# Optimization experiments

Hardware: AMD Instinct MI355X
Metric: run time of the kernel (lower is better)

The kernel has to match this reference:

```python
import jax, jax.numpy as jnp
import numpy as np

N, C, NUM_IDS = 4096, 2048, 256


def setup_inputs() -> dict:
    key = jax.random.key(0)
    k1, k2 = jax.random.split(key)
    x = jax.random.normal(k1, (N, C), dtype=jnp.float32)
    target = jax.random.randint(k2, (N,), 0, NUM_IDS, dtype=jnp.int64)
    return {
        "input": x,
        "target": target,
        "hyper_paramter": 1,
        "usemean": 1,
        "use_exp": 0,
    }


def _pair_stats(x, W):
    """Vectorized sum over lower-tri pairs (i>j) weighted by W (lower-triangular 0/1).

    cov = sum_{i>j} W_ij (x_i - x_j)(x_i - x_j)^T = X^T (diag(S 1) - S) X, S = W + W^T
    vec = sum_{i>j} W_ij (x_i - x_j)       = X^T (rowsum(W) - colsum(W))
    """
    S = W + W.T                       # [N, N] symmetric pair mask
    d = S.sum(axis=1)                 # degree
    Lx = d[:, None] * x - S @ x       # (diag(d) - S) @ X, [N, C]
    cov = x.T @ Lx                    # [C, C]
    vec = x.T @ (W.sum(axis=1) - W.sum(axis=0))  # [C]
    return cov, vec, W.sum()


def reference(input, target, hyper_paramter, usemean, use_exp):
    x = input
    same_id = (target[:, None] == target[None, :])
    pos_l = jnp.tril(same_id.astype(x.dtype), -1)          # positive pairs, i>j
    neg_l = jnp.tril((~same_id).astype(x.dtype), -1)       # negative pairs, i>j

    cov_i, sum_i, npos = _pair_stats(x, pos_l)
    cov_j, sum_j, nneg = _pair_stats(x, neg_l)

    norm_i = jnp.linalg.norm(cov_i)
    norm_j = jnp.linalg.norm(cov_j)

    if use_exp:
        dist = jnp.exp(-jnp.linalg.norm(cov_i - cov_j))
        loss = dist
    else:
        # original broadcasts zeros(C) + diff(C,1) -> (C,C) matrix of identical
        # columns; its Frobenius norm = sqrt(C) * norm(column vector)
        mean_norm = jnp.sqrt(jnp.asarray(x.shape[1], x.dtype)) * jnp.linalg.norm(
            sum_i / npos - sum_j / nneg
        )
        dist = norm_i - hyper_paramter * norm_j - usemean * mean_norm
        loss = jnp.maximum(dist, 0.0)
    return (loss, dist, norm_i, norm_j)
```

## Files before the change

### kernel.cpp

```cpp
#include <hip/hip_runtime.h>
#include <math.h>


#define N_ROWS 4096
#define C_DIM  2048
#define NCLS   256
#define RLCAP  96
#define NRB    17
#define NKS    32
#define TSB    16384
#define SLOT_B 32768

typedef __attribute__((ext_vector_type(4))) float f32x4;
typedef __attribute__((ext_vector_type(2))) long v2i64;

__device__ __forceinline__ void gload16(const void* g, void* l) {
    __builtin_amdgcn_global_load_lds(
        (const __attribute__((address_space(1))) unsigned int*)g,
        (__attribute__((address_space(3))) unsigned int*)l, 16, 0, 0);
}

__device__ __forceinline__ int pk4_fp8(float a, float b, float c, float d) {
    int r = __builtin_amdgcn_cvt_pk_fp8_f32(a, b, 0, false);
    r = __builtin_amdgcn_cvt_pk_fp8_f32(c, d, r, true);
    return r;
}

__global__ __launch_bounds__(256) void k_scan_conv(
    const int* __restrict__ t, const float* __restrict__ x,
    float* __restrict__ ca, float* __restrict__ cb,
    float* __restrict__ dr, float* __restrict__ nposf,
    unsigned char* __restrict__ xbf) {
    __shared__ int ts[N_ROWS];
    __shared__ int rl[RLCAP];
    __shared__ int cnt_s;
    int a = blockIdx.x, tid = threadIdx.x;
    for (int i = tid; i < N_ROWS; i += 256) ts[i] = t[i];
    __syncthreads();
    if (tid < 64) {
        int lane = tid;
        unsigned long long ltmask = (1ULL << lane) - 1ULL;
        int base = 0;
        for (int i0 = 0; i0 < N_ROWS; i0 += 64) {
            int i = i0 + lane;
            bool m = (ts[i] == a);
            unsigned long long mask = __ballot(m);
            if (m) {
                int r = base + (int)__popcll(mask & ltmask);
                if (r < RLCAP) rl[r] = i;
            }
            base += (int)__popcll(mask);
        }
        if (lane == 0) {
            cnt_s = base;
            float cf = (float)base;
            atomicAdd(nposf, 0.5f * cf * (cf - 1.f));
        }
        int cc = base < RLCAP ? base : RLCAP;
        for (int r = lane; r < cc; r += 64) {
            int i = rl[r];
            ca[i] = (float)(2 * r - base + 1);
            cb[i] = (float)(2 * i - 2 * r + base - N_ROWS);
            dr[i] = (float)base;
        }
    }
    __syncthreads();
    int cnt = cnt_s < RLCAP ? cnt_s : RLCAP;
    int c0 = tid * 4, c1 = 1024 + tid * 4;
    float s0=0,s1=0,s2=0,s3=0,s4=0,s5=0,s6=0,s7=0;
    int ks0 = c0 >> 6, cc0 = c0 & 63;
    int ks1 = c1 >> 6, cc1 = c1 & 63;
    int sl0 = (cc0 & 31) >> 3, ch0 = cc0 >> 5, b0 = cc0 & 7;
    int sl1 = (cc1 & 31) >> 3, ch1 = cc1 >> 5, b1 = cc1 & 7;
    for (int r = 0; r < cnt; ++r) {
        int i = rl[r];
        const float* row = x + (size_t)i * C_DIM;
        float4 v0 = *(const float4*)(row + c0);
        float4 v1 = *(const float4*)(row + c1);
        s0+=v0.x; s1+=v0.y; s2+=v0.z; s3+=v0.w;
        s4+=v1.x; s5+=v1.y; s6+=v1.z; s7+=v1.w;
        int rb2 = i >> 8, rr = i & 255;
        unsigned char* tb = xbf + (size_t)rb2 * NKS * TSB;
        int w0 = pk4_fp8(v0.x, v0.y, v0.z, v0.w);
        int w1 = pk4_fp8(v1.x, v1.y, v1.z, v1.w);
        int sz = (rr >> 1) & 3;
        *(int*)(tb + (size_t)ks0 * TSB + rr * 64 + (((sl0 ^ sz) << 4) + (ch0 << 3) + b0)) = w0;
        *(int*)(tb + (size_t)ks1 * TSB + rr * 64 + (((sl1 ^ sz) << 4) + (ch1 << 3) + b1)) = w1;
    }
    unsigned char* tbg = xbf + (size_t)16 * NKS * TSB;
    int g0 = pk4_fp8(s0, s1, s2, s3);
    int g1 = pk4_fp8(s4, s5, s6, s7);
    int sza = (a >> 1) & 3;
    *(int*)(tbg + (size_t)ks0 * TSB + a * 64 + (((sl0 ^ sza) << 4) + (ch0 << 3) + b0)) = g0;
    *(int*)(tbg + (size_t)ks1 * TSB + a * 64 + (((sl1 ^ sza) << 4) + (ch1 << 3) + b1)) = g1;
}

__device__ __forceinline__ v2i64 frag16(const unsigned char* buf, int row0,
                                        int lane) {
    int r = row0 + (lane & 15);
    int s = lane >> 4;
    return *(const v2i64*)(buf + r * 64 + ((s ^ ((r >> 1) & 3)) << 4));
}

__global__ __launch_bounds__(1024, 4) void k_gram(
    const unsigned char* __restrict__ xbf, const float* __restrict__ dr,
    const float* __restrict__ ca, const float* __restrict__ cb,
    const float* __restrict__ nposf, float* __restrict__ ssq) {
    const int nwg = NRB * (NRB + 1) / 2;
    int orig = blockIdx.x;
    int q8 = nwg >> 3, r8 = nwg & 7;
    int xcd = orig & 7, loc = orig >> 3;
    int b = (xcd < r8 ? xcd * (q8 + 1) : r8 * (q8 + 1) + (xcd - r8) * q8) + loc;
    int bi = 0;
    while (b >= NRB - bi) { b -= NRB - bi; ++bi; }
    int bj = bi + b;
    bool diag = (bi == bj);
    bool needRS = (bj == NRB - 1);

    __shared__ __align__(16) unsigned char Sl[4][SLOT_B];
    __shared__ float drow[256], dcol[256], urow[256], ucol[256];
    __shared__ float rsum[256];
    __shared__ float wred[16 * 16];

    int tid = threadIdx.x;
    int lane = tid & 63;
    int w = tid >> 6;
    int wr4 = w >> 2;
    int wc4 = w & 3;

    const unsigned char* abase = xbf + (size_t)bi * NKS * TSB;
    const unsigned char* bbase = xbf + (size_t)bj * NKS * TSB;
    int off0 = w * 1024 + lane * 16;

#pragma unroll
    for (int p = 0; p < 2; ++p) {
        gload16(abase + (size_t)p * TSB + off0, Sl[p] + off0);
        gload16(bbase + (size_t)p * TSB + off0, Sl[p] + 16384 + off0);
    }
    if (tid < 256) {
        float np = nposf[0];
        float inp = 1.f / np;
        float inn = 1.f / (0.5f * (float)N_ROWS * ((float)N_ROWS - 1.f) - np);
        int gi = bi * 256 + tid;
        bool vi = gi < N_ROWS;
        drow[tid] = vi ? dr[gi] : 0.f;
        urow[tid] = vi ? (ca[gi] * inp - cb[gi] * inn) : 0.f;
        int gj = bj * 256 + tid;
        bool vj = gj < N_ROWS;
        dcol[tid] = vj ? dr[gj] : 0.f;
        ucol[tid] = vj ? (ca[gj] * inp - cb[gj] * inn) : 0.f;
        rsum[tid] = 0.f;
    }

    f32x4 acc[4][4] = {};
    __syncthreads();

#define STAGE_STEP(ks)                                                         \
    {                                                                          \
        unsigned char* sl = Sl[(ks) & 3];                                      \
        gload16(abase + (size_t)(ks) * TSB + off0, sl + off0);                 \
        gload16(bbase + (size_t)(ks) * TSB + off0, sl + 16384 + off0);         \
    }

#define COMPUTE_STEP(t)                                                        \
    {                                                                          \
        const unsigned char* sb = Sl[(t) & 3];                                 \
        v2i64 A[4], B[4];                                                      \
        _Pragma("unroll")                                                      \
        for (int m = 0; m < 4; ++m) A[m] = frag16(sb, wr4 * 64 + m * 16, lane);\
        _Pragma("unroll")                                                      \
        for (int n = 0; n < 4; ++n) B[n] = frag16(sb + 16384, wc4 * 64 + n * 16, lane);\
        __builtin_amdgcn_s_setprio(1);                                         \
        _Pragma("unroll")                                                      \
        for (int m = 0; m < 4; ++m)                                            \
            _Pragma("unroll")                                                  \
            for (int n = 0; n < 4; ++n) {                                      \
                acc[m][n] = __builtin_amdgcn_mfma_f32_16x16x32_fp8_fp8(        \
                    A[m][0], B[n][0], acc[m][n], 0, 0, 0);                     \
                acc[m][n] = __builtin_amdgcn_mfma_f32_16x16x32_fp8_fp8(        \
                    A[m][1], B[n][1], acc[m][n], 0, 0, 0);                     \
            }                                                                  \
        __builtin_amdgcn_s_setprio(0);                                         \
    }

    for (int t = 0; t < NKS - 2; ++t) {
        STAGE_STEP(t + 2);
        asm volatile("s_waitcnt vmcnt(4)" ::: "memory");
        asm volatile("s_barrier" ::: "memory");
        COMPUTE_STEP(t);
    }
    asm volatile("s_waitcnt vmcnt(2)" ::: "memory");
    asm volatile("s_barrier" ::: "memory");
    COMPUTE_STEP(NKS - 2);
    asm volatile("s_waitcnt vmcnt(0)" ::: "memory");
    asm volatile("s_barrier" ::: "memory");
    COMPUTE_STEP(NKS - 1);

    float fK = diag ? 1.f : 2.f;
    float vs[7] = {0,0,0,0,0,0,0};
#pragma unroll
    for (int m = 0; m < 4; ++m) {
#pragma unroll
        for (int qq = 0; qq < 4; ++qq) {
            int iw = wr4 * 64 + m * 16 + (lane >> 4) * 4 + qq;
            int gi = bi * 256 + iw;
            float di = drow[iw];
            float ui = urow[iw];
            bool iX = gi < N_ROWS;
            float rs = 0.f;
#pragma unroll
            for (int n = 0; n < 4; ++n) {
                int jw = wc4 * 64 + n * 16 + (lane & 15);
                int gj = bj * 256 + jw;
                float dj = dcol[jw];
                float k = acc[m][n][qq];
                float k2 = k * k;
                bool jX = gj < N_ROWS;
                if (iX && jX) {
                    vs[0] += fK * k2;
                    vs[1] += 0.5f * fK * (di + dj) * k2;
                    vs[2] += fK * di * dj * k2;
                    vs[6] += fK * ui * ucol[jw] * k;
                } else if (iX) {
                    vs[3] += k2;
                    vs[4] += di * k2;
                } else if (!jX) {
                    vs[5] += fK * k2;
                }
                if (needRS) rs += k;
            }
            if (needRS) {
                rs += __shfl_xor(rs, 1);
                rs += __shfl_xor(rs, 2);
                rs += __shfl_xor(rs, 4);
                rs += __shfl_xor(rs, 8);
                if ((lane & 15) == 0) atomicAdd(&rsum[iw], rs);
            }
        }
    }
#pragma unroll
    for (int v = 0; v < 7; ++v) {
        float xv = vs[v];
        for (int off = 32; off; off >>= 1) xv += __shfl_down(xv, off);
        if (lane == 0) wred[w * 16 + v] = xv;
    }
    __syncthreads();
    if (tid < 7) {
        float sum = 0.f;
#pragma unroll
        for (int ww = 0; ww < 16; ++ww) sum += wred[ww * 16 + tid];
        atomicAdd(ssq + (tid == 6 ? 10 : tid), sum);
    }
    if (needRS && tid < 256) {
        float r = rsum[tid];
        float a6 = diag ? 0.f : r * r;
        float a7 = diag ? 0.f : drow[tid] * r * r;
        float a8 = diag ? r * r : 0.f;
        float a9 = diag ? r : 0.f;
        for (int off = 32; off; off >>= 1) {
            a6 += __shfl_down(a6, off);
            a7 += __shfl_down(a7, off);
            a8 += __shfl_down(a8, off);
            a9 += __shfl_down(a9, off);
        }
        if (lane == 0) {
            atomicAdd(ssq + 6, a6);
            atomicAdd(ssq + 7, a7);
            atomicAdd(ssq + 8, a8);
            atomicAdd(ssq + 9, a9);
        }
    }
#undef STAGE_STEP
#undef COMPUTE_STEP
}

__global__ void k_final(const float* __restrict__ ssq, const float* __restrict__ nposf,
                        const int* __restrict__ hyper, const int* __restrict__ usemean,
                        const int* __restrict__ use_exp, float* __restrict__ out) {
    if (threadIdx.x != 0) return;
    double S0 = ssq[0], S1 = ssq[1], S2 = ssq[2], R2 = ssq[3], PG = ssq[4];
    double Q2 = ssq[5], TS = ssq[6], PS = ssq[7], GS = ssq[8], SS = ssq[9];
    double U2 = ssq[10];
    double Nf = (double)N_ROWS;
    double ni2 = S2 - 2.0 * PG + Q2;
    double nj2 = Nf * Nf * S0 + S2 + SS * SS + Q2 - 2.0 * Nf * S1
               - 2.0 * Nf * TS + 2.0 * Nf * R2 + 2.0 * PS - 2.0 * PG - 2.0 * GS;
    double trAB = Nf * S1 - S2 - PS + 2.0 * PG - Nf * R2 + GS - Q2;
    double d2 = ni2 - 2.0 * trAB + nj2;
    float norm_i = (float)sqrt(fmax(ni2, 0.0));
    float norm_j = (float)sqrt(fmax(nj2, 0.0));
    float h = (float)hyper[0], um = (float)usemean[0];
    float loss, dist;
    if (use_exp[0]) {
        dist = (float)exp(-sqrt(fmax(d2, 0.0)));
        loss = dist;
    } else {
        float mean_norm = sqrtf((float)C_DIM) * sqrtf(fmaxf((float)U2, 0.f));
        dist = norm_i - h * norm_j - um * mean_norm;
        loss = fmaxf(dist, 0.f);
    }
    out[0] = loss; out[1] = dist; out[2] = norm_i; out[3] = norm_j;
}

extern "C" void kernel_launch(void* const* d_in, const int* in_sizes, int n_in,
                              void* d_out, int out_size, void* d_ws, size_t ws_size,
                              hipStream_t stream) {
    const float* x = (const float*)d_in[0];
    const int* t = (const int*)d_in[1];
    const int* hyper = (const int*)d_in[2];
    const int* usemean = (const int*)d_in[3];
    const int* use_exp = (const int*)d_in[4];
    float* out = (float*)d_out;

    unsigned char* xbf = (unsigned char*)d_ws;
    size_t xbf_bytes = (size_t)NRB * NKS * TSB;
    float* ca    = (float*)(xbf + xbf_bytes);
    float* cb    = ca + N_ROWS;
    float* dr    = cb + N_ROWS;
    float* ssq   = dr + N_ROWS;
    float* nposf = ssq + 16;

    hipMemsetAsync(ssq, 0, 32 * sizeof(float), stream);

    k_scan_conv<<<NCLS, 256, 0, stream>>>(t, x, ca, cb, dr, nposf, xbf);
    k_gram<<<NRB * (NRB + 1) / 2, 1024, 0, stream>>>(xbf, dr, ca, cb, nposf, ssq);
    k_final<<<1, 64, 0, stream>>>(ssq, nposf, hyper, usemean, use_exp, out);
}
```

Baseline: 79.97 us.

## Split class scan and fp8 conversion into separate kernels with doubled row parallelism

The fused scan+convert kernel is split into a single-wave scan kernel that writes per-class row lists to global memory, a conversion kernel that uses two blocks per class and processes alternating rows, and a small kernel that sums the two partial class sums and packs them to fp8. This doubles the block count for the memory-bound fp32-to-fp8 conversion and drops the 256-thread staging of all targets into shared memory. The cost is two extra kernel launches and a global round trip for the row lists and partial sums.

Result: slower. 96.69 us (+20.9%).

```diff
diff --git a/kernel.cpp b/kernel.cpp
--- a/kernel.cpp
+++ b/kernel.cpp
@@ -26,54 +26,54 @@
     return r;
 }
 
-__global__ __launch_bounds__(256) void k_scan_conv(
-    const int* __restrict__ t, const float* __restrict__ x,
-    float* __restrict__ ca, float* __restrict__ cb,
-    float* __restrict__ dr, float* __restrict__ nposf,
+__global__ __launch_bounds__(64) void k_scan(
+    const int* __restrict__ t, int* __restrict__ counts,
+    int* __restrict__ rowlist, float* __restrict__ ca, float* __restrict__ cb,
+    float* __restrict__ dr, float* __restrict__ nposf) {
+    __shared__ int rl[RLCAP];
+    int a = blockIdx.x;
+    int lane = threadIdx.x;
+    unsigned long long ltmask = (1ULL << lane) - 1ULL;
+    int base = 0;
+    for (int i0 = 0; i0 < N_ROWS; i0 += 64) {
+        int i = i0 + lane;
+        bool m = (t[i] == a);
+        unsigned long long mask = __ballot(m);
+        if (m) {
+            int r = base + (int)__popcll(mask & ltmask);
+            if (r < RLCAP) { rl[r] = i; rowlist[a * RLCAP + r] = i; }
+        }
+        base += (int)__popcll(mask);
+    }
+    if (lane == 0) {
+        counts[a] = base;
+        float cf = (float)base;
+        atomicAdd(nposf, 0.5f * cf * (cf - 1.f));
+    }
+    __syncthreads();
+    int cc = base < RLCAP ? base : RLCAP;
+    for (int r = lane; r < cc; r += 64) {
+        int i = rl[r];
+        ca[i] = (float)(2 * r - base + 1);
+        cb[i] = (float)(2 * i - 2 * r + base - N_ROWS);
+        dr[i] = (float)base;
+    }
+}
+
+__global__ __launch_bounds__(256) void k_conv2(
+    const float* __restrict__ x, const int* __restrict__ counts,
+    const int* __restrict__ rowlist, float* __restrict__ gpart,
     unsigned char* __restrict__ xbf) {
-    __shared__ int ts[N_ROWS];
-    __shared__ int rl[RLCAP];
-    __shared__ int cnt_s;
-    int a = blockIdx.x, tid = threadIdx.x;
-    for (int i = tid; i < N_ROWS; i += 256) ts[i] = t[i];
-    __syncthreads();
-    if (tid < 64) {
-        int lane = tid;
-        unsigned long long ltmask = (1ULL << lane) - 1ULL;
-        int base = 0;
-        for (int i0 = 0; i0 < N_ROWS; i0 += 64) {
-            int i = i0 + lane;
-            bool m = (ts[i] == a);
-            unsigned long long mask = __ballot(m);
-            if (m) {
-                int r = base + (int)__popcll(mask & ltmask);
-                if (r < RLCAP) rl[r] = i;
-            }
-            base += (int)__popcll(mask);
-        }
-        if (lane == 0) {
-            cnt_s = base;
-            float cf = (float)base;
-            atomicAdd(nposf, 0.5f * cf * (cf - 1.f));
-        }
-        int cc = base < RLCAP ? base : RLCAP;
-        for (int r = lane; r < cc; r += 64) {
-            int i = rl[r];
-            ca[i] = (float)(2 * r - base + 1);
-            cb[i] = (float)(2 * i - 2 * r + base - N_ROWS);
-            dr[i] = (float)base;
-        }
-    }
-    __syncthreads();
-    int cnt = cnt_s < RLCAP ? cnt_s : RLCAP;
+    int a = blockIdx.x >> 1, h = blockIdx.x & 1, tid = threadIdx.x;
+    int cnt = counts[a]; if (cnt > RLCAP) cnt = RLCAP;
     int c0 = tid * 4, c1 = 1024 + tid * 4;
     float s0=0,s1=0,s2=0,s3=0,s4=0,s5=0,s6=0,s7=0;
     int ks0 = c0 >> 6, cc0 = c0 & 63;
     int ks1 = c1 >> 6, cc1 = c1 & 63;
     int sl0 = (cc0 & 31) >> 3, ch0 = cc0 >> 5, b0 = cc0 & 7;
     int sl1 = (cc1 & 31) >> 3, ch1 = cc1 >> 5, b1 = cc1 & 7;
-    for (int r = 0; r < cnt; ++r) {
-        int i = rl[r];
+    for (int r = h; r < cnt; r += 2) {
+        int i = rowlist[a * RLCAP + r];
         const float* row = x + (size_t)i * C_DIM;
         float4 v0 = *(const float4*)(row + c0);
         float4 v1 = *(const float4*)(row + c1);
@@ -87,10 +87,29 @@
         *(int*)(tb + (size_t)ks0 * TSB + rr * 64 + (((sl0 ^ sz) << 4) + (ch0 << 3) + b0)) = w0;
         *(int*)(tb + (size_t)ks1 * TSB + rr * 64 + (((sl1 ^ sz) << 4) + (ch1 << 3) + b1)) = w1;
     }
+    float* gp = gpart + (size_t)(a * 2 + h) * C_DIM;
+    *(float4*)(gp + c0) = make_float4(s0, s1, s2, s3);
+    *(float4*)(gp + c1) = make_float4(s4, s5, s6, s7);
+}
+
+__global__ __launch_bounds__(256) void k_gfin(
+    const float* __restrict__ gpart, unsigned char* __restrict__ xbf) {
+    int a = blockIdx.x, tid = threadIdx.x;
+    int c0 = tid * 4, c1 = 1024 + tid * 4;
+    const float* p0 = gpart + (size_t)(a * 2) * C_DIM;
+    const float* p1 = gpart + (size_t)(a * 2 + 1) * C_DIM;
+    float4 u0 = *(const float4*)(p0 + c0);
+    float4 u1 = *(const float4*)(p1 + c0);
+    float4 w0 = *(const float4*)(p0 + c1);
+    float4 w1 = *(const float4*)(p1 + c1);
+    int g0 = pk4_fp8(u0.x + u1.x, u0.y + u1.y, u0.z + u1.z, u0.w + u1.w);
+    int g1 = pk4_fp8(w0.x + w1.x, w0.y + w1.y, w0.z + w1.z, w0.w + w1.w);
+    int ks0 = c0 >> 6, cc0 = c0 & 63;
+    int ks1 = c1 >> 6, cc1 = c1 & 63;
+    int sl0 = (cc0 & 31) >> 3, ch0 = cc0 >> 5, b0 = cc0 & 7;
+    int sl1 = (cc1 & 31) >> 3, ch1 = cc1 >> 5, b1 = cc1 & 7;
+    int sza = (a >> 1) & 3;
     unsigned char* tbg = xbf + (size_t)16 * NKS * TSB;
-    int g0 = pk4_fp8(s0, s1, s2, s3);
-    int g1 = pk4_fp8(s4, s5, s6, s7);
-    int sza = (a >> 1) & 3;
     *(int*)(tbg + (size_t)ks0 * TSB + a * 64 + (((sl0 ^ sza) << 4) + (ch0 << 3) + b0)) = g0;
     *(int*)(tbg + (size_t)ks1 * TSB + a * 64 + (((sl1 ^ sza) << 4) + (ch1 << 3) + b1)) = g1;
 }
@@ -319,10 +338,15 @@
     float* dr    = cb + N_ROWS;
     float* ssq   = dr + N_ROWS;
     float* nposf = ssq + 16;
+    float* gpart = nposf + 15;
+    int* counts  = (int*)(gpart + (size_t)2 * NCLS * C_DIM);
+    int* rowlist = counts + NCLS;
 
     hipMemsetAsync(ssq, 0, 32 * sizeof(float), stream);
 
-    k_scan_conv<<<NCLS, 256, 0, stream>>>(t, x, ca, cb, dr, nposf, xbf);
+    k_scan<<<NCLS, 64, 0, stream>>>(t, counts, rowlist, ca, cb, dr, nposf);
+    k_conv2<<<NCLS * 2, 256, 0, stream>>>(x, counts, rowlist, gpart, xbf);
+    k_gfin<<<NCLS, 256, 0, stream>>>(gpart, xbf);
     k_gram<<<NRB * (NRB + 1) / 2, 1024, 0, stream>>>(xbf, dr, ca, cb, nposf, ssq);
     k_final<<<1, 64, 0, stream>>>(ssq, nposf, hyper, usemean, use_exp, out);
 }
```
